# Performance work log

Hardware: AMD Instinct MI355X
Metric: run time of the kernel (lower is better)

Reference implementation:

```python
import jax, jax.numpy as jnp
import numpy as np

KW = 3          # kernel_width
PAD = (KW - 1) // 2


def setup_inputs() -> dict:
    key = jax.random.key(0)
    ks = jax.random.split(key, 7)
    B, Lq, Lk, D, C = 8, 1024, 1024, 512, 512  # D=q_size, C=k_size
    return {
        "q": jax.random.normal(ks[0], (B, Lq, D), jnp.float32),
        "k": jax.random.normal(ks[1], (B, Lk, C), jnp.float32),
        "W_kernel": jax.random.normal(ks[2], (D, C * KW), jnp.float32) * (1.0 / np.sqrt(D)),
        "b_kernel": jax.random.normal(ks[3], (C * KW,), jnp.float32) * 0.02,
        "W_bias": jax.random.normal(ks[4], (D, 1), jnp.float32) * (1.0 / np.sqrt(D)),
        "b_bias": jax.random.normal(ks[5], (1,), jnp.float32) * 0.02,
        "bias_b": jax.random.normal(ks[6], (1,), jnp.float32),
    }


def reference(q, k, W_kernel, b_kernel, W_bias, b_bias, bias_b):
    B, Lq, D = q.shape
    _, Lk, C = k.shape
    # per-(batch, query) dynamic conv kernels: [B, Lq, C, KW]
    kernel = (q @ W_kernel + b_kernel).reshape(B, Lq, C, KW)
    # per-(batch, query) scalar bias: [B, Lq]
    bias = (q @ W_bias + b_bias)[..., 0]
    # windowed view of k (cross-correlation with 'same' padding)
    kpad = jnp.pad(k, ((0, 0), (PAD, PAD), (0, 0)))  # [B, Lk+2*PAD, C]
    win_idx = jnp.arange(Lk)[:, None] + jnp.arange(KW)[None, :]  # [Lk, KW]
    kwin = kpad[:, win_idx, :]  # [B, Lk, KW, C]
    # a[b,i,j] = sum_{c,w} kernel[b,i,c,w] * kpad[b, j+w, c] + bias[b,i] + bias_b
    a_ij = jnp.einsum('bicw,bjwc->bij', kernel, kwin)
    return a_ij + bias[:, :, None] + bias_b
```

## Files before the change

kernel.cpp:

```cpp
#include <hip/hip_runtime.h>


typedef __attribute__((ext_vector_type(8))) short s8vec;
typedef __attribute__((ext_vector_type(4))) float floatx4;

__device__ __forceinline__ unsigned short f2bf(float f) {
    union { float f; unsigned u; } v; v.f = f;
    unsigned r = (v.u + 0x7FFFu + ((v.u >> 16) & 1u)) >> 16;
    return (unsigned short)r;
}

__device__ __forceinline__ void gl2lds16(const void* g, void* l) {
    __builtin_amdgcn_global_load_lds(
        (__attribute__((address_space(1))) void*)(g),
        (__attribute__((address_space(3))) void*)(l), 16, 0, 0);
}

__global__ void cvt_all(const float* __restrict__ q, const float* __restrict__ k,
                        unsigned short* __restrict__ qbf, unsigned short* __restrict__ kp,
                        const float* __restrict__ Wb, const float* __restrict__ b_bias,
                        float* __restrict__ biasb,
                        const float* __restrict__ W, unsigned short* __restrict__ Wt) {
    int blk = blockIdx.x;
    if (blk < 4104) {
        int t = blk * 256 + threadIdx.x;
        if (t < 524288) {
            const float4* p = (const float4*)q + 2 * (size_t)t;
            float4 a = p[0], b = p[1];
            union { unsigned short s[8]; uint4 v; } o;
            o.s[0]=f2bf(a.x); o.s[1]=f2bf(a.y); o.s[2]=f2bf(a.z); o.s[3]=f2bf(a.w);
            o.s[4]=f2bf(b.x); o.s[5]=f2bf(b.y); o.s[6]=f2bf(b.z); o.s[7]=f2bf(b.w);
            ((uint4*)qbf)[t] = o.v;
        } else if (t < 1048576) {
            int e8 = t - 524288;
            size_t e = (size_t)e8 * 8;
            int b = e8 >> 16;
            int j = (e8 >> 6) & 1023;
            int c = (e8 & 63) * 8;
            const float4* p = (const float4*)(k + e);
            float4 a = p[0], bb = p[1];
            union { unsigned short s[8]; uint4 v; } o;
            o.s[0]=f2bf(a.x); o.s[1]=f2bf(a.y); o.s[2]=f2bf(a.z); o.s[3]=f2bf(a.w);
            o.s[4]=f2bf(bb.x); o.s[5]=f2bf(bb.y); o.s[6]=f2bf(bb.z); o.s[7]=f2bf(bb.w);
            *(uint4*)(kp + ((size_t)(b * 1028 + j + 1) * 512 + c)) = o.v;
        } else if (t < 1050624) {
            int z = t - 1048576;
            int b = z >> 8, r = (z >> 6) & 3, ch = z & 63;
            int row = r ? (1024 + r) : 0;
            *(uint4*)(kp + ((size_t)(b * 1028 + row) * 512 + ch * 8)) = make_uint4(0u,0u,0u,0u);
        }
    } else if (blk < 6152) {
        int row  = (blk - 4104) * 4 + (threadIdx.x >> 6);
        int lane = threadIdx.x & 63;
        const float4* qr = (const float4*)(q + (size_t)row * 512) + lane * 2;
        const float4* wb = (const float4*)Wb + lane * 2;
        float4 a0 = qr[0], a1 = qr[1], b0 = wb[0], b1 = wb[1];
        float s = a0.x*b0.x + a0.y*b0.y + a0.z*b0.z + a0.w*b0.w
                + a1.x*b1.x + a1.y*b1.y + a1.z*b1.z + a1.w*b1.w;
        #pragma unroll
        for (int off = 32; off > 0; off >>= 1) s += __shfl_down(s, off);
        if (lane == 0) biasb[row] = s + b_bias[0];
    } else {
        __shared__ float lds[32][33];
        int p = blk - 6152;
        int cw0 = (p % 48) * 32, d0 = (p / 48) * 32;
        int tid = threadIdx.x;
        #pragma unroll
        for (int rep = 0; rep < 4; rep++) {
            int e = rep * 256 + tid, dy = e >> 5, dx = e & 31;
            lds[dy][dx] = W[(size_t)(d0 + dy) * 1536 + cw0 + dx];
        }
        __syncthreads();
        #pragma unroll
        for (int rep = 0; rep < 4; rep++) {
            int e = rep * 256 + tid, cy = e >> 5, cx = e & 31;
            int cw = cw0 + cy, c = cw / 3, w = cw % 3;
            Wt[((size_t)(w * 512 + c)) * 512 + d0 + cx] = f2bf(lds[cx][cy]);
        }
    }
}

__global__ __launch_bounds__(128) void gemm_A(const unsigned short* __restrict__ Abf,
                                              const unsigned short* __restrict__ Bbf,
                                              const float* __restrict__ b_kernel,
                                              unsigned short* __restrict__ G) {
    __shared__ unsigned short lds_a[64 * 64];
    __shared__ unsigned short lds_b[128 * 64];
    int g = blockIdx.x;
    int xcd = g & 7, slot = g >> 3;
    int i_blk = xcd * 16 + (slot & 15);
    int n_blk = slot >> 4;
    int i0 = i_blk * 64, n0 = n_blk * 128;
    int tid = threadIdx.x, wid = tid >> 6, lane = tid & 63;
    floatx4 acc[4][4] = {};

    for (int kk = 0; kk < 512; kk += 64) {
        #pragma unroll
        for (int s = 0; s < 12; ++s) {
            int t = s * 2 + wid;
            if (t < 8) {
                const unsigned short* ga = Abf + (size_t)(i0 + t * 8 + (lane >> 3)) * 512 + kk + (lane & 7) * 8;
                gl2lds16(ga, (char*)lds_a + t * 1024);
            } else {
                int u = t - 8;
                const unsigned short* gb = Bbf + (size_t)(n0 + u * 8 + (lane >> 3)) * 512 + kk + (lane & 7) * 8;
                gl2lds16(gb, (char*)lds_b + u * 1024);
            }
        }
        __syncthreads();
        int ra = lane & 15, q8 = (lane >> 4) * 8;
        #pragma unroll
        for (int h = 0; h < 2; ++h) {
            s8vec af[4], bf_[4];
            #pragma unroll
            for (int mi = 0; mi < 4; mi++)
                af[mi] = *(const s8vec*)(lds_a + (mi * 16 + ra) * 64 + h * 32 + q8);
            #pragma unroll
            for (int ni = 0; ni < 4; ni++)
                bf_[ni] = *(const s8vec*)(lds_b + (wid * 64 + ni * 16 + ra) * 64 + h * 32 + q8);
            #pragma unroll
            for (int mi = 0; mi < 4; mi++)
                #pragma unroll
                for (int ni = 0; ni < 4; ni++)
                    acc[mi][ni] = __builtin_amdgcn_mfma_f32_16x16x32_bf16(af[mi], bf_[ni], acc[mi][ni], 0, 0, 0);
        }
        __syncthreads();
    }

    int cl = lane & 15, qd = lane >> 4;
    #pragma unroll
    for (int mi = 0; mi < 4; mi++) {
        #pragma unroll
        for (int ni = 0; ni < 4; ni++) {
            int n_all = n0 + wid * 64 + ni * 16 + cl;
            int c = n_all & 511, w = n_all >> 9;
            float bk = b_kernel[c * 3 + w];
            #pragma unroll
            for (int r = 0; r < 4; r++) {
                int i_g = i0 + mi * 16 + qd * 4 + r;
                int b = i_g >> 10, ii = i_g & 1023;
                G[((size_t)((b * 3 + w) * 1024 + ii)) * 512 + c] = f2bf(acc[mi][ni][r] + bk);
            }
        }
    }
}

__global__ __launch_bounds__(128) void gemm_B(const unsigned short* __restrict__ G,
                                              const unsigned short* __restrict__ kp,
                                              const float* __restrict__ biasb,
                                              const float* __restrict__ bias_b,
                                              float* __restrict__ out) {
    __shared__ unsigned short lds_a[3 * 64 * 32];
    __shared__ unsigned short lds_k[144 * 32];
    int g = blockIdx.x;
    int b = g & 7, slot = g >> 3;
    int j0 = (slot & 7) * 128;
    int i0 = (slot >> 3) * 64;
    int tid = threadIdx.x, wid = tid >> 6, lane = tid & 63;
    floatx4 acc[4][4] = {};
    const unsigned short* Gb  = G  + (size_t)b * 3 * 1024 * 512;
    const unsigned short* kpb = kp + (size_t)b * 1028 * 512;
    float bb = bias_b[0];

    for (int kk = 0; kk < 512; kk += 32) {
        #pragma unroll
        for (int s = 0; s < 11; ++s) {
            int t = s * 2 + wid;
            if (t < 21) {
                if (t < 12) {
                    int w = t >> 2, chunk = t & 3;
                    const unsigned short* ga = Gb + (size_t)(w * 1024 + i0 + chunk * 16 + (lane >> 2)) * 512
                                                  + kk + (lane & 3) * 8;
                    gl2lds16(ga, (char*)lds_a + t * 1024);
                } else {
                    int u = t - 12;
                    const unsigned short* gk = kpb + (size_t)(j0 + u * 16 + (lane >> 2)) * 512
                                                   + kk + (lane & 3) * 8;
                    gl2lds16(gk, (char*)lds_k + u * 1024);
                }
            }
        }
        __syncthreads();
        int ra = lane & 15, q8 = (lane >> 4) * 8;
        #pragma unroll
        for (int w = 0; w < 3; ++w) {
            s8vec af[4], bfr[4];
            #pragma unroll
            for (int mi = 0; mi < 4; mi++)
                af[mi] = *(const s8vec*)(lds_a + (w * 64 + mi * 16 + ra) * 32 + q8);
            #pragma unroll
            for (int ni = 0; ni < 4; ni++) {
                int rr = wid * 64 + ni * 16 + ra + w;
                bfr[ni] = *(const s8vec*)(lds_k + rr * 32 + q8);
            }
            #pragma unroll
            for (int mi = 0; mi < 4; mi++)
                #pragma unroll
                for (int ni = 0; ni < 4; ni++)
                    acc[mi][ni] = __builtin_amdgcn_mfma_f32_16x16x32_bf16(af[mi], bfr[ni], acc[mi][ni], 0, 0, 0);
        }
        __syncthreads();
    }

    int cl = lane & 15, qd = lane >> 4;
    #pragma unroll
    for (int mi = 0; mi < 4; mi++) {
        #pragma unroll
        for (int r = 0; r < 4; r++) {
            int i_loc = mi * 16 + qd * 4 + r;
            float bv = biasb[b * 1024 + i0 + i_loc] + bb;
            #pragma unroll
            for (int ni = 0; ni < 4; ni++) {
                int j_loc = wid * 64 + ni * 16 + cl;
                out[((size_t)(b * 1024 + i0 + i_loc)) * 1024 + j0 + j_loc] = acc[mi][ni][r] + bv;
            }
        }
    }
}

extern "C" void kernel_launch(void* const* d_in, const int* in_sizes, int n_in,
                              void* d_out, int out_size, void* d_ws, size_t ws_size,
                              hipStream_t stream) {
    const float* q        = (const float*)d_in[0];
    const float* k        = (const float*)d_in[1];
    const float* W_kernel = (const float*)d_in[2];
    const float* b_kernel = (const float*)d_in[3];
    const float* W_bias   = (const float*)d_in[4];
    const float* b_bias   = (const float*)d_in[5];
    const float* bias_b   = (const float*)d_in[6];
    float* out = (float*)d_out;

    char* ws = (char*)d_ws;
    unsigned short* q_bf = (unsigned short*)(ws);
    unsigned short* kp   = (unsigned short*)(ws + 8388608);
    unsigned short* Wt   = (unsigned short*)(ws + 8388608 + 8421376 + 16384);
    unsigned short* G    = (unsigned short*)(ws + 8388608 + 8421376 + 16384 + 1572864);
    float*          bsb  = (float*)(ws + 8388608 + 8421376 + 16384 + 1572864 + 25165824);

    cvt_all<<<6920, 256, 0, stream>>>(q, k, q_bf, kp, W_bias, b_bias, bsb, W_kernel, Wt);
    gemm_A<<<1536, 128, 0, stream>>>(q_bf, Wt, b_kernel, G);
    gemm_B<<<1024, 128, 0, stream>>>(G, kp, bsb, bias_b, out);
}
```

Measured before the change: 152.9 us.

## Split gemm_B reduction over channels with atomic accumulation and wider j tiles

gemm_B now uses 256-thread blocks covering 256 output columns, and splits the 512-channel reduction into two halves whose partial sums are added into the output with unsafeAtomicAdd. A new out_init kernel pre-fills the output with the per-row bias so the atomics can accumulate onto it. This aims to raise per-block work and reuse of the G tile across more columns while keeping enough blocks. The cost is an extra full write of the 32MB output plus atomic read-modify-write traffic, and the summation order is no longer fixed.

```diff
diff --git a/kernel.cpp b/kernel.cpp
--- a/kernel.cpp
+++ b/kernel.cpp
@@ -80,6 +80,17 @@
     }
 }
 
+__global__ void out_init(const float* __restrict__ biasb, const float* __restrict__ bias_b,
+                         float* __restrict__ out) {
+    int t = blockIdx.x * 256 + threadIdx.x;
+    int row = t >> 5;
+    float v = biasb[row] + bias_b[0];
+    float4 vv = make_float4(v, v, v, v);
+    float4* dst = (float4*)(out + (size_t)row * 1024) + (t & 31) * 8;
+    #pragma unroll
+    for (int r = 0; r < 8; r++) dst[r] = vv;
+}
+
 __global__ __launch_bounds__(128) void gemm_A(const unsigned short* __restrict__ Abf,
                                               const unsigned short* __restrict__ Bbf,
                                               const float* __restrict__ b_kernel,
@@ -137,7 +148,7 @@
             float bk = b_kernel[c * 3 + w];
             #pragma unroll
             for (int r = 0; r < 4; r++) {
-                int i_g = i0 + mi * 16 + qd * 4 + r;
+                int i_g = i0 + wid * 0 + mi * 16 + qd * 4 + r;
                 int b = i_g >> 10, ii = i_g & 1023;
                 G[((size_t)((b * 3 + w) * 1024 + ii)) * 512 + c] = f2bf(acc[mi][ni][r] + bk);
             }
@@ -145,28 +156,27 @@
     }
 }
 
-__global__ __launch_bounds__(128) void gemm_B(const unsigned short* __restrict__ G,
+__global__ __launch_bounds__(256) void gemm_B(const unsigned short* __restrict__ G,
                                               const unsigned short* __restrict__ kp,
-                                              const float* __restrict__ biasb,
-                                              const float* __restrict__ bias_b,
                                               float* __restrict__ out) {
     __shared__ unsigned short lds_a[3 * 64 * 32];
-    __shared__ unsigned short lds_k[144 * 32];
+    __shared__ unsigned short lds_k[272 * 32];
     int g = blockIdx.x;
-    int b = g & 7, slot = g >> 3;
-    int j0 = (slot & 7) * 128;
-    int i0 = (slot >> 3) * 64;
+    int b = g & 7, s = g >> 3;
+    int kh = s & 1;
+    int j0 = ((s >> 1) & 3) * 256;
+    int i0 = (s >> 3) * 64;
     int tid = threadIdx.x, wid = tid >> 6, lane = tid & 63;
     floatx4 acc[4][4] = {};
     const unsigned short* Gb  = G  + (size_t)b * 3 * 1024 * 512;
     const unsigned short* kpb = kp + (size_t)b * 1028 * 512;
-    float bb = bias_b[0];
-
-    for (int kk = 0; kk < 512; kk += 32) {
-        #pragma unroll
-        for (int s = 0; s < 11; ++s) {
-            int t = s * 2 + wid;
-            if (t < 21) {
+    int k_beg = kh * 256;
+
+    for (int kk = k_beg; kk < k_beg + 256; kk += 32) {
+        #pragma unroll
+        for (int s2 = 0; s2 < 8; ++s2) {
+            int t = s2 * 4 + wid;
+            if (t < 29) {
                 if (t < 12) {
                     int w = t >> 2, chunk = t & 3;
                     const unsigned short* ga = Gb + (size_t)(w * 1024 + i0 + chunk * 16 + (lane >> 2)) * 512
@@ -208,11 +218,11 @@
         #pragma unroll
         for (int r = 0; r < 4; r++) {
             int i_loc = mi * 16 + qd * 4 + r;
-            float bv = biasb[b * 1024 + i0 + i_loc] + bb;
+            float* orow = out + ((size_t)(b * 1024 + i0 + i_loc)) * 1024 + j0;
             #pragma unroll
             for (int ni = 0; ni < 4; ni++) {
                 int j_loc = wid * 64 + ni * 16 + cl;
-                out[((size_t)(b * 1024 + i0 + i_loc)) * 1024 + j0 + j_loc] = acc[mi][ni][r] + bv;
+                unsafeAtomicAdd(&orow[j_loc], acc[mi][ni][r]);
             }
         }
     }
@@ -238,6 +248,7 @@
     float*          bsb  = (float*)(ws + 8388608 + 8421376 + 16384 + 1572864 + 25165824);
 
     cvt_all<<<6920, 256, 0, stream>>>(q, k, q_bf, kp, W_bias, b_bias, bsb, W_kernel, Wt);
+    out_init<<<1024, 256, 0, stream>>>(bsb, bias_b, out);
     gemm_A<<<1536, 128, 0, stream>>>(q_bf, Wt, b_kernel, G);
-    gemm_B<<<1024, 128, 0, stream>>>(G, kp, bsb, bias_b, out);
-}
+    gemm_B<<<1024, 256, 0, stream>>>(G, kp, out);
+}
```

Result: slower. 204.6 us (+33.8%).

## Enlarge GEMM tiles to 256-thread blocks in both projection and correlation kernels

Applied to the files above, without the earlier changes.

gemm_A moves from 64x128 tiles with 2 waves and K-step 64 to 128x128 tiles with 4 waves in a 2x2 layout and K-step 32. gemm_B widens its j tile from 128 to 256 with 4 waves, so each block loads a 272-row k window once and shares the G tile across more columns. Both changes aim to cut redundant global/LDS traffic per MFMA and halve the block count. The trade-off is fewer blocks (768 and 512) for 256 CUs, a smaller K step in gemm_A that needs more barriers, and a larger LDS footprint in gemm_B.

```diff
diff --git a/kernel.cpp b/kernel.cpp
--- a/kernel.cpp
+++ b/kernel.cpp
@@ -80,50 +80,45 @@
     }
 }
 
-__global__ __launch_bounds__(128) void gemm_A(const unsigned short* __restrict__ Abf,
+__global__ __launch_bounds__(256) void gemm_A(const unsigned short* __restrict__ Abf,
                                               const unsigned short* __restrict__ Bbf,
                                               const float* __restrict__ b_kernel,
                                               unsigned short* __restrict__ G) {
-    __shared__ unsigned short lds_a[64 * 64];
-    __shared__ unsigned short lds_b[128 * 64];
+    __shared__ unsigned short lds_a[128 * 32];
+    __shared__ unsigned short lds_b[128 * 32];
     int g = blockIdx.x;
     int xcd = g & 7, slot = g >> 3;
-    int i_blk = xcd * 16 + (slot & 15);
-    int n_blk = slot >> 4;
-    int i0 = i_blk * 64, n0 = n_blk * 128;
+    int n_blk = slot / 8;
+    int i_blk = xcd * 8 + (slot & 7);
+    int i0 = i_blk * 128;
+    int n0 = n_blk * 128;
     int tid = threadIdx.x, wid = tid >> 6, lane = tid & 63;
+    int wm = wid >> 1, wn = wid & 1;
     floatx4 acc[4][4] = {};
 
-    for (int kk = 0; kk < 512; kk += 64) {
-        #pragma unroll
-        for (int s = 0; s < 12; ++s) {
-            int t = s * 2 + wid;
-            if (t < 8) {
-                const unsigned short* ga = Abf + (size_t)(i0 + t * 8 + (lane >> 3)) * 512 + kk + (lane & 7) * 8;
-                gl2lds16(ga, (char*)lds_a + t * 1024);
-            } else {
-                int u = t - 8;
-                const unsigned short* gb = Bbf + (size_t)(n0 + u * 8 + (lane >> 3)) * 512 + kk + (lane & 7) * 8;
-                gl2lds16(gb, (char*)lds_b + u * 1024);
-            }
+    for (int kk = 0; kk < 512; kk += 32) {
+        #pragma unroll
+        for (int s = 0; s < 2; ++s) {
+            int t = wid * 2 + s;
+            const unsigned short* ga = Abf + (size_t)(i0 + t * 16 + (lane >> 2)) * 512 + kk + (lane & 3) * 8;
+            gl2lds16(ga, (char*)lds_a + t * 1024);
+            const unsigned short* gb = Bbf + (size_t)(n0 + t * 16 + (lane >> 2)) * 512 + kk + (lane & 3) * 8;
+            gl2lds16(gb, (char*)lds_b + t * 1024);
         }
         __syncthreads();
         int ra = lane & 15, q8 = (lane >> 4) * 8;
-        #pragma unroll
-        for (int h = 0; h < 2; ++h) {
-            s8vec af[4], bf_[4];
-            #pragma unroll
-            for (int mi = 0; mi < 4; mi++)
-                af[mi] = *(const s8vec*)(lds_a + (mi * 16 + ra) * 64 + h * 32 + q8);
+        s8vec af[4], bf_[4];
+        #pragma unroll
+        for (int mi = 0; mi < 4; mi++)
+            af[mi] = *(const s8vec*)(lds_a + (wm * 64 + mi * 16 + ra) * 32 + q8);
+        #pragma unroll
+        for (int ni = 0; ni < 4; ni++)
+            bf_[ni] = *(const s8vec*)(lds_b + (wn * 64 + ni * 16 + ra) * 32 + q8);
+        #pragma unroll
+        for (int mi = 0; mi < 4; mi++)
             #pragma unroll
             for (int ni = 0; ni < 4; ni++)
-                bf_[ni] = *(const s8vec*)(lds_b + (wid * 64 + ni * 16 + ra) * 64 + h * 32 + q8);
-            #pragma unroll
-            for (int mi = 0; mi < 4; mi++)
-                #pragma unroll
-                for (int ni = 0; ni < 4; ni++)
-                    acc[mi][ni] = __builtin_amdgcn_mfma_f32_16x16x32_bf16(af[mi], bf_[ni], acc[mi][ni], 0, 0, 0);
-        }
+                acc[mi][ni] = __builtin_amdgcn_mfma_f32_16x16x32_bf16(af[mi], bf_[ni], acc[mi][ni], 0, 0, 0);
         __syncthreads();
     }
 
@@ -132,12 +127,12 @@
     for (int mi = 0; mi < 4; mi++) {
         #pragma unroll
         for (int ni = 0; ni < 4; ni++) {
-            int n_all = n0 + wid * 64 + ni * 16 + cl;
+            int n_all = n0 + wn * 64 + ni * 16 + cl;
             int c = n_all & 511, w = n_all >> 9;
             float bk = b_kernel[c * 3 + w];
             #pragma unroll
             for (int r = 0; r < 4; r++) {
-                int i_g = i0 + mi * 16 + qd * 4 + r;
+                int i_g = i0 + wm * 64 + mi * 16 + qd * 4 + r;
                 int b = i_g >> 10, ii = i_g & 1023;
                 G[((size_t)((b * 3 + w) * 1024 + ii)) * 512 + c] = f2bf(acc[mi][ni][r] + bk);
             }
@@ -145,17 +140,17 @@
     }
 }
 
-__global__ __launch_bounds__(128) void gemm_B(const unsigned short* __restrict__ G,
+__global__ __launch_bounds__(256) void gemm_B(const unsigned short* __restrict__ G,
                                               const unsigned short* __restrict__ kp,
                                               const float* __restrict__ biasb,
                                               const float* __restrict__ bias_b,
                                               float* __restrict__ out) {
     __shared__ unsigned short lds_a[3 * 64 * 32];
-    __shared__ unsigned short lds_k[144 * 32];
+    __shared__ unsigned short lds_k[272 * 32];
     int g = blockIdx.x;
     int b = g & 7, slot = g >> 3;
-    int j0 = (slot & 7) * 128;
-    int i0 = (slot >> 3) * 64;
+    int j0 = (slot & 3) * 256;
+    int i0 = (slot >> 2) * 64;
     int tid = threadIdx.x, wid = tid >> 6, lane = tid & 63;
     floatx4 acc[4][4] = {};
     const unsigned short* Gb  = G  + (size_t)b * 3 * 1024 * 512;
@@ -164,9 +159,9 @@
 
     for (int kk = 0; kk < 512; kk += 32) {
         #pragma unroll
-        for (int s = 0; s < 11; ++s) {
-            int t = s * 2 + wid;
-            if (t < 21) {
+        for (int s2 = 0; s2 < 8; ++s2) {
+            int t = s2 * 4 + wid;
+            if (t < 29) {
                 if (t < 12) {
                     int w = t >> 2, chunk = t & 3;
                     const unsigned short* ga = Gb + (size_t)(w * 1024 + i0 + chunk * 16 + (lane >> 2)) * 512
@@ -209,10 +204,11 @@
         for (int r = 0; r < 4; r++) {
             int i_loc = mi * 16 + qd * 4 + r;
             float bv = biasb[b * 1024 + i0 + i_loc] + bb;
+            float* orow = out + ((size_t)(b * 1024 + i0 + i_loc)) * 1024 + j0;
             #pragma unroll
             for (int ni = 0; ni < 4; ni++) {
                 int j_loc = wid * 64 + ni * 16 + cl;
-                out[((size_t)(b * 1024 + i0 + i_loc)) * 1024 + j0 + j_loc] = acc[mi][ni][r] + bv;
+                orow[j_loc] = acc[mi][ni][r] + bv;
             }
         }
     }
@@ -238,6 +234,6 @@
     float*          bsb  = (float*)(ws + 8388608 + 8421376 + 16384 + 1572864 + 25165824);
 
     cvt_all<<<6920, 256, 0, stream>>>(q, k, q_bf, kp, W_bias, b_bias, bsb, W_kernel, Wt);
-    gemm_A<<<1536, 128, 0, stream>>>(q_bf, Wt, b_kernel, G);
-    gemm_B<<<1024, 128, 0, stream>>>(G, kp, bsb, bias_b, out);
-}
+    gemm_A<<<768, 256, 0, stream>>>(q_bf, Wt, b_kernel, G);
+    gemm_B<<<512, 256, 0, stream>>>(G, kp, bsb, bias_b, out);
+}
```

After: 142.5 us. 6.8% less time.
